# Performance work log

Hardware: AMD Instinct MI355X
Metric: run time of the kernel (lower is better)

Reference implementation:

```python
import jax, jax.numpy as jnp
import numpy as np
import math

GROUPS = 32
HEADS = 8
EPS_GN = 1e-5


def group_norm(x, w, b):
    # x: [B, C, H, W]; GroupNorm32 computes in float32
    B, C, H, W = x.shape
    xg = x.astype(jnp.float32).reshape(B, GROUPS, C // GROUPS, H, W)
    mu = xg.mean(axis=(2, 3, 4), keepdims=True)
    var = xg.var(axis=(2, 3, 4), keepdims=True)
    xn = (xg - mu) * jax.lax.rsqrt(var + EPS_GN)
    xn = xn.reshape(B, C, H, W)
    return (xn * w[None, :, None, None] + b[None, :, None, None]).astype(x.dtype)


def fresnel_interference(H, W, wavelength):
    ys, xs = jnp.meshgrid(jnp.arange(H, dtype=jnp.float32),
                          jnp.arange(W, dtype=jnp.float32), indexing='ij')
    pos = jnp.stack([ys, xs], axis=-1).reshape(-1, 2)  # [N, 2]
    diff = pos[None, :, :] - pos[:, None, :]           # [N, N, 2]
    dist = jnp.sqrt((diff ** 2).sum(-1) + 1e-8)        # [N, N]
    phase = 2.0 * math.pi * dist / (jnp.abs(wavelength) * H + 1e-6)
    return jnp.cos(phase)


def fresnel_attn(h, qkv_w, out_w, out_b, wavelength):
    B, C, H, W = h.shape
    N = H * W
    dh = C // HEADS
    scale = dh ** -0.5
    xf = h.reshape(B, C, N).transpose(0, 2, 1)                 # [B, N, C]
    qkv = xf @ qkv_w                                            # [B, N, 3C]
    q, k, v = jnp.split(qkv, 3, axis=-1)
    def heads(t):
        return t.reshape(B, N, HEADS, dh).transpose(0, 2, 1, 3)  # [B, Hh, N, dh]
    q, k, v = heads(q), heads(k), heads(v)
    dots = jnp.einsum('bhnd,bhmd->bhnm', q, k) * scale
    interference = fresnel_interference(H, W, wavelength)       # [N, N]
    dots = dots + interference[None, None] * 0.1
    attn = jax.nn.softmax(dots, axis=-1)
    out = jnp.einsum('bhnm,bhmd->bhnd', attn, v)
    out = out.transpose(0, 2, 1, 3).reshape(B, N, C)
    out = out @ out_w + out_b
    return out.transpose(0, 2, 1).reshape(B, C, H, W)


def cross_attn(h, context, q_w, k_w, v_w, out_w, out_b):
    B, C, H, W = h.shape
    N = H * W
    inner = q_w.shape[1]
    dh = inner // HEADS
    scale = dh ** -0.5
    xf = h.reshape(B, C, N).transpose(0, 2, 1)                 # [B, N, C]
    q = xf @ q_w                                                # [B, N, inner]
    k = context @ k_w                                           # [B, L, inner]
    v = context @ v_w
    L = context.shape[1]
    q = q.reshape(B, N, HEADS, dh).transpose(0, 2, 1, 3)
    k = k.reshape(B, L, HEADS, dh).transpose(0, 2, 1, 3)
    v = v.reshape(B, L, HEADS, dh).transpose(0, 2, 1, 3)
    attn = jax.nn.softmax(jnp.einsum('bhnd,bhld->bhnl', q, k) * scale, axis=-1)
    out = jnp.einsum('bhnl,bhld->bhnd', attn, v)
    out = out.transpose(0, 2, 1, 3).reshape(B, N, inner)
    out = out @ out_w + out_b
    return out.transpose(0, 2, 1).reshape(B, C, H, W)


def setup_inputs() -> dict:
    key = jax.random.key(0)
    ks = jax.random.split(key, 10)
    B, C, H, W = 4, 512, 32, 32
    ctx_len, ctx_dim = 77, 768
    s = lambda d: 1.0 / math.sqrt(d)
    return {
        'x': jax.random.normal(ks[0], (B, C, H, W), jnp.float32),
        'context': jax.random.normal(ks[1], (B, ctx_len, ctx_dim), jnp.float32),
        'gn1_w': jnp.ones((C,), jnp.float32),
        'gn1_b': jnp.zeros((C,), jnp.float32),
        'gn2_w': jnp.ones((C,), jnp.float32),
        'gn2_b': jnp.zeros((C,), jnp.float32),
        'fa_qkv_w': jax.random.normal(ks[2], (C, 3 * C), jnp.float32) * s(C),
        'fa_out_w': jax.random.normal(ks[3], (C, C), jnp.float32) * s(C),
        'fa_out_b': jnp.zeros((C,), jnp.float32),
        'wavelength': jnp.asarray(0.1, jnp.float32),
        'ca_q_w': jax.random.normal(ks[4], (C, 512), jnp.float32) * s(C),
        'ca_k_w': jax.random.normal(ks[5], (ctx_dim, 512), jnp.float32) * s(ctx_dim),
        'ca_v_w': jax.random.normal(ks[6], (ctx_dim, 512), jnp.float32) * s(ctx_dim),
        'ca_out_w': jax.random.normal(ks[7], (512, C), jnp.float32) * s(512),
        'ca_out_b': jnp.zeros((C,), jnp.float32),
    }


def reference(x, context, gn1_w, gn1_b, gn2_w, gn2_b,
              fa_qkv_w, fa_out_w, fa_out_b, wavelength,
              ca_q_w, ca_k_w, ca_v_w, ca_out_w, ca_out_b):
    h = group_norm(x, gn1_w, gn1_b)
    h = fresnel_attn(h, fa_qkv_w, fa_out_w, fa_out_b, wavelength)
    x = x + h
    h = group_norm(x, gn2_w, gn2_b)
    h = cross_attn(h, context, ca_q_w, ca_k_w, ca_v_w, ca_out_w, ca_out_b)
    return x + h
```

## Files before the change

kernel.cpp:

```cpp
#include <hip/hip_runtime.h>
#include <hip/hip_bf16.h>
#include <math.h>

#define B_    4
#define N_    1024
#define L_    77

typedef float f4 __attribute__((ext_vector_type(4)));
typedef short bf8 __attribute__((ext_vector_type(8)));
typedef short s4v __attribute__((ext_vector_type(4)));

#if __has_builtin(__builtin_amdgcn_exp2f)
#define EXP2(x) __builtin_amdgcn_exp2f(x)
#else
#define EXP2(x) exp2f(x)
#endif

typedef const __attribute__((address_space(1))) void* gas_t;
typedef __attribute__((address_space(3))) void* las_t;
#define GLL16(g, l) __builtin_amdgcn_global_load_lds((gas_t)(const void*)(g), (las_t)(void*)(l), 16, 0, 0)

__device__ __forceinline__ float fs(short s) {
    unsigned u = ((unsigned)(unsigned short)s) << 16;
    return __builtin_bit_cast(float, u);
}
__device__ __forceinline__ short sf(float f) {
    unsigned u = __builtin_bit_cast(unsigned, f);
    unsigned r = (u + 0x7FFF + ((u >> 16) & 1)) >> 16;
    return (short)r;
}
__device__ __forceinline__ bf8 zero8() { bf8 v; for (int i = 0; i < 8; ++i) v[i] = 0; return v; }
__device__ __forceinline__ f4 zerof4() { f4 v; for (int i = 0; i < 4; ++i) v[i] = 0.f; return v; }

#define MFMA(a, b, c) __builtin_amdgcn_mfma_f32_16x16x32_bf16((a), (b), (c), 0, 0, 0)

__device__ __forceinline__ void gn_body(const float* __restrict__ src,
                                        const float* __restrict__ w,
                                        const float* __restrict__ bs,
                                        short* __restrict__ dst, int g, int b)
{
    const float* xb = src + ((size_t)b * 512 + g * 16) * 1024;
    float s = 0.f, ss = 0.f;
    for (int l = threadIdx.x; l < 4096; l += 256) {
        float4 v = *(const float4*)(xb + l * 4);
        s += v.x + v.y + v.z + v.w;
        ss += v.x * v.x + v.y * v.y + v.z * v.z + v.w * v.w;
    }
    for (int off = 32; off; off >>= 1) {
        s  += __shfl_down(s,  off);
        ss += __shfl_down(ss, off);
    }
    __shared__ float sred[8], ssred[8];
    int wid = threadIdx.x >> 6;
    if ((threadIdx.x & 63) == 0) { sred[wid] = s; ssred[wid] = ss; }
    __syncthreads();
    if (threadIdx.x == 0) {
        float S = 0.f, SS = 0.f;
        for (int i = 0; i < 4; ++i) { S += sred[i]; SS += ssred[i]; }
        float mu = S * (1.f / 16384.f);
        float var = SS * (1.f / 16384.f) - mu * mu;
        sred[4] = mu; ssred[4] = rsqrtf(var + 1e-5f);
    }
    __syncthreads();
    float mu = sred[4], rs = ssred[4];

    int c4 = threadIdx.x & 3, nb = threadIdx.x >> 2;
    int c = g * 16 + c4 * 4;
    float4 wv = *(const float4*)(w + c);
    float4 bv = *(const float4*)(bs + c);
    for (int rep = 0; rep < 16; ++rep) {
        int n = rep * 64 + nb;
        float v0 = xb[(size_t)(c4 * 4 + 0) * 1024 + n];
        float v1 = xb[(size_t)(c4 * 4 + 1) * 1024 + n];
        float v2 = xb[(size_t)(c4 * 4 + 2) * 1024 + n];
        float v3 = xb[(size_t)(c4 * 4 + 3) * 1024 + n];
        s4v hb;
        hb[0] = sf((v0 - mu) * rs * wv.x + bv.x);
        hb[1] = sf((v1 - mu) * rs * wv.y + bv.y);
        hb[2] = sf((v2 - mu) * rs * wv.z + bv.z);
        hb[3] = sf((v3 - mu) * rs * wv.w + bv.w);
        *(s4v*)(dst + ((size_t)b * 1024 + n) * 512 + c) = hb;
    }
}

__device__ __forceinline__ void wtile(const float* __restrict__ in, short* __restrict__ out,
                                      int K, int J, int tile, int tid, float (*t)[33])
{
    int jt = J >> 5;
    int j0 = (tile % jt) * 32, k0 = (tile / jt) * 32;
    int tx = tid & 31, ty = tid >> 5;
#pragma unroll
    for (int i = 0; i < 4; ++i)
        t[ty + i * 8][tx] = in[(size_t)(k0 + ty + i * 8) * J + j0 + tx];
    __syncthreads();
#pragma unroll
    for (int i = 0; i < 4; ++i)
        out[(size_t)(j0 + ty + i * 8) * K + k0 + tx] = sf(t[tx][ty + i * 8]);
}

__global__ __launch_bounds__(256)
void prep_mega(const float* __restrict__ x, const float* __restrict__ gn1w,
               const float* __restrict__ gn1b, short* __restrict__ h1b,
               const float* __restrict__ wl, short* __restrict__ tab,
               float* __restrict__ gstat,
               const float* __restrict__ qkvw, short* __restrict__ qkvwT,
               const float* __restrict__ faow, short* __restrict__ faowT,
               const float* __restrict__ caqw, short* __restrict__ caqwT,
               const float* __restrict__ cakw, short* __restrict__ cakwT,
               const float* __restrict__ cavw, short* __restrict__ cavwT,
               const float* __restrict__ caow, short* __restrict__ caowT,
               const float* __restrict__ ctx, short* __restrict__ ctxb)
{
    __shared__ float tls[32][33];
    int bid = blockIdx.x, tid = threadIdx.x;
    if (bid < 128) { gn_body(x, gn1w, gn1b, h1b, bid & 31, bid >> 5); return; }
    bid -= 128;
    if (bid < 16) {
        if (bid == 0) gstat[tid] = 0.f;
        int idx = bid * 256 + tid;
        if (idx < 3969) {
            int i = idx / 63, j = idx - i * 63;
            float dy = (float)(i - 31), dx = (float)(j - 31);
            float dist = sqrtf(dy * dy + dx * dx + 1e-8f);
            float den = fabsf(wl[0]) * 32.0f + 1e-6f;
            tab[idx] = sf(0.1f * cosf(6.283185307179586f * dist / den) * 1.4426950408889634f);
        }
        return;
    }
    bid -= 16;
    if (bid < 768) { wtile(qkvw, qkvwT, 512, 1536, bid, tid, tls); return; }
    bid -= 768;
    if (bid < 256) { wtile(faow, faowT, 512, 512, bid, tid, tls); return; }
    bid -= 256;
    if (bid < 256) { wtile(caqw, caqwT, 512, 512, bid, tid, tls); return; }
    bid -= 256;
    if (bid < 384) { wtile(cakw, cakwT, 768, 512, bid, tid, tls); return; }
    bid -= 384;
    if (bid < 384) { wtile(cavw, cavwT, 768, 512, bid, tid, tls); return; }
    bid -= 384;
    if (bid < 256) { wtile(caow, caowT, 512, 512, bid, tid, tls); return; }
    bid -= 256;
    int base = bid * 1024 + tid * 4;
    float4 v = *(const float4*)(ctx + base);
    s4v o; o[0] = sf(v.x); o[1] = sf(v.y); o[2] = sf(v.z); o[3] = sf(v.w);
    *(s4v*)(ctxb + base) = o;
}

template<int EPI>
__device__ __forceinline__ void gemm_body(
    short* As, short* Ws, int j0, int m0, int b,
    const short* __restrict__ A, const short* __restrict__ Wt,
    const float* __restrict__ bias, const float* __restrict__ res,
    void* __restrict__ outv, void* __restrict__ out2v, float* __restrict__ gstat,
    int M, int K, int J, long aStride, long wStride, long oStride, long o2Stride)
{
    int tid = threadIdx.x, w = tid >> 6, lane = tid & 63;
    int lr = lane & 15, lg = lane >> 4;
    int wr = w >> 1, wc = w & 1;
    const short* Ab  = A  + (size_t)b * aStride;
    const short* Wtb = Wt + (size_t)b * wStride;

    int srow = lane >> 2, schk = (lane & 3) * 8;
    const short* agp  = Ab  + (size_t)(m0 + w * 16 + srow) * K + schk;
    const short* wgp0 = Wtb + (size_t)(j0 + w * 32 + srow) * K + schk;
    const short* wgp1 = Wtb + (size_t)(j0 + w * 32 + 16 + srow) * K + schk;
    short* alp  = As + w * 512;
    short* wlp0 = Ws + w * 1024;
    short* wlp1 = Ws + w * 1024 + 512;

    f4 acc[2][4];
#pragma unroll
    for (int i = 0; i < 2; ++i)
#pragma unroll
        for (int j = 0; j < 4; ++j) acc[i][j] = zerof4();

    GLL16(agp,  alp);
    GLL16(wgp0, wlp0);
    GLL16(wgp1, wlp1);
    __syncthreads();

    int nk = K >> 5;
    for (int t = 0; t < nk; ++t) {
        int bb = t & 1, nb2 = bb ^ 1;
        if (t + 1 < nk) {
            int ko = (t + 1) << 5;
            GLL16(agp + ko,  alp + nb2 * 2048);
            GLL16(wgp0 + ko, wlp0 + nb2 * 4096);
            GLL16(wgp1 + ko, wlp1 + nb2 * 4096);
        }
        bf8 af[2], bfr[4];
#pragma unroll
        for (int fi = 0; fi < 2; ++fi)
            af[fi] = *(const bf8*)(As + bb * 2048 + (wr * 32 + fi * 16 + lr) * 32 + lg * 8);
#pragma unroll
        for (int fj = 0; fj < 4; ++fj)
            bfr[fj] = *(const bf8*)(Ws + bb * 4096 + (wc * 64 + fj * 16 + lr) * 32 + lg * 8);
#pragma unroll
        for (int fi = 0; fi < 2; ++fi)
#pragma unroll
            for (int fj = 0; fj < 4; ++fj)
                acc[fi][fj] = MFMA(af[fi], bfr[fj], acc[fi][fj]);
        __syncthreads();
    }

    if (EPI == 1 || EPI == 2) {
        float* out = (float*)outv + (size_t)b * oStride;
        const float* rp = res + (size_t)b * oStride;
#pragma unroll
        for (int fi = 0; fi < 2; ++fi) {
            int mbase = m0 + wr * 32 + fi * 16 + lg * 4;
            float4 bq = *(const float4*)(bias + mbase);
            float bvr[4] = {bq.x, bq.y, bq.z, bq.w};
            float sg = 0.f, ssg = 0.f;
#pragma unroll
            for (int reg = 0; reg < 4; ++reg) {
                size_t ro = (size_t)(mbase + reg) * J + j0 + wc * 64;
#pragma unroll
                for (int fj = 0; fj < 4; ++fj) {
                    size_t idx = ro + fj * 16 + lr;
                    float v = acc[fi][fj][reg] + bvr[reg] + rp[idx];
                    out[idx] = v;
                    if (EPI == 2) { sg += v; ssg += v * v; }
                }
            }
            if (EPI == 2) {
#pragma unroll
                for (int off = 32; off; off >>= 1) {
                    sg  += __shfl_down(sg,  off);
                    ssg += __shfl_down(ssg, off);
                }
                if (lane == 0) {
                    int g = mbase >> 4;
                    atomicAdd(&gstat[b * 64 + g * 2], sg);
                    atomicAdd(&gstat[b * 64 + g * 2 + 1], ssg);
                }
            }
        }
    } else if (EPI == 3) {
        if (j0 < 1024) {
            short* out = (short*)outv + (size_t)b * oStride;
#pragma unroll
            for (int fi = 0; fi < 2; ++fi)
#pragma unroll
                for (int reg = 0; reg < 4; ++reg) {
                    int m = m0 + wr * 32 + fi * 16 + lg * 4 + reg;
#pragma unroll
                    for (int fj = 0; fj < 4; ++fj)
                        out[(size_t)m * 1024 + j0 + wc * 64 + fj * 16 + lr] = sf(acc[fi][fj][reg]);
                }
        } else {
            short* Vgp = (short*)out2v + (size_t)b * o2Stride;
#pragma unroll
            for (int fi = 0; fi < 2; ++fi) {
                int n = m0 + wr * 32 + fi * 16 + lg * 4;
#pragma unroll
                for (int fj = 0; fj < 4; ++fj) {
                    int dg = j0 - 1024 + wc * 64 + fj * 16 + lr;
                    s4v v;
#pragma unroll
                    for (int reg = 0; reg < 4; ++reg) v[reg] = sf(acc[fi][fj][reg]);
                    *(s4v*)(Vgp + (size_t)dg * 1024 + n) = v;
                }
            }
        }
    } else {
        if (j0 < 512) {
            short* out = (short*)outv + (size_t)b * oStride;
#pragma unroll
            for (int fi = 0; fi < 2; ++fi)
#pragma unroll
                for (int reg = 0; reg < 4; ++reg) {
                    int m = m0 + wr * 32 + fi * 16 + lg * 4 + reg;
                    if (m < M) {
#pragma unroll
                        for (int fj = 0; fj < 4; ++fj)
                            out[(size_t)m * 512 + j0 + wc * 64 + fj * 16 + lr] = sf(acc[fi][fj][reg]);
                    }
                }
        } else {
            short* vt = (short*)out2v + (size_t)b * o2Stride;
#pragma unroll
            for (int fi = 0; fi < 2; ++fi) {
                int l0 = m0 + wr * 32 + fi * 16 + lg * 4;
                if (l0 < 80) {
#pragma unroll
                    for (int fj = 0; fj < 4; ++fj) {
                        int dg = j0 - 512 + wc * 64 + fj * 16 + lr;
                        s4v v;
#pragma unroll
                        for (int reg = 0; reg < 4; ++reg) v[reg] = sf(acc[fi][fj][reg]);
                        *(s4v*)(vt + (size_t)dg * 80 + l0) = v;
                    }
                }
            }
        }
    }
}

template<int EPI>
__global__ __launch_bounds__(256)
void gemm_std(const short* __restrict__ A, const short* __restrict__ Wt,
              const float* __restrict__ bias, const float* __restrict__ res,
              void* __restrict__ outv, void* __restrict__ out2v, float* __restrict__ gstat,
              int M, int K, int J, long aStride, long wStride, long oStride, long o2Stride)
{
    __shared__ short As[2 * 64 * 32];
    __shared__ short Ws[2 * 128 * 32];
    gemm_body<EPI>(As, Ws, blockIdx.x * 128, blockIdx.y * 64, blockIdx.z,
                   A, Wt, bias, res, outv, out2v, gstat, M, K, J,
                   aStride, wStride, oStride, o2Stride);
}

__global__ __launch_bounds__(256)
void gemm_qkv_kv(const short* __restrict__ h1b, const short* __restrict__ qkvwT,
                 short* __restrict__ qkb, short* __restrict__ Vg,
                 const short* __restrict__ ctxb, const short* __restrict__ cakwT,
                 short* __restrict__ k2b, short* __restrict__ v2t)
{
    __shared__ short As[2 * 64 * 32];
    __shared__ short Ws[2 * 128 * 32];
    if (blockIdx.y < 16) {
        gemm_body<3>(As, Ws, blockIdx.x * 128, blockIdx.y * 64, blockIdx.z,
                     h1b, qkvwT, nullptr, nullptr, qkb, Vg, nullptr,
                     1024, 512, 1536, 524288L, 0L, 1048576L, 524288L);
    } else if (blockIdx.x < 8) {
        gemm_body<4>(As, Ws, blockIdx.x * 128, (blockIdx.y - 16) * 64, blockIdx.z,
                     ctxb, cakwT, nullptr, nullptr, k2b, v2t, nullptr,
                     77, 768, 1024, 59136L, 0L, 39424L, 40960L);
    }
}

__global__ __launch_bounds__(256)
void fresnel_attn_v3(const short* __restrict__ qkb, const short* __restrict__ Vg,
                     const short* __restrict__ tab, short* __restrict__ ao)
{
    int qb = blockIdx.x, h = blockIdx.y, b = blockIdx.z;
    int n0 = qb * 64;
    __shared__ short Ks[2][64][64];
    __shared__ short Vt[2][64][64];
    __shared__ short Ps[4][16][72];
    __shared__ short tabs[4032];
    int tid = threadIdx.x, w = tid >> 6, lane = tid & 63;
    int lr = lane & 15, lg = lane >> 4;
    const short* qp = qkb + (size_t)b * 1048576;
    const short* vp = Vg + ((size_t)b * 512 + h * 64) * 1024;

    for (int l = tid; l < 504; l += 256)
        *(bf8*)&tabs[l * 8] = *(const bf8*)(tab + l * 8);

    int q = n0 + w * 16 + lr;
    bf8 qf0 = *(const bf8*)(qp + (size_t)q * 1024 + h * 64 + lg * 8);
    bf8 qf1 = *(const bf8*)(qp + (size_t)q * 1024 + h * 64 + 32 + lg * 8);

    int sr0 = tid >> 3, sc0 = tid & 7;
    int sr1 = 32 + sr0;
    int sw0 = ((sc0 ^ (sr0 & 7))) * 8;
    int sw1 = ((sc0 ^ (sr1 & 7))) * 8;

    *(bf8*)&Ks[0][sr0][sw0] = *(const bf8*)(qp + (size_t)sr0 * 1024 + 512 + h * 64 + sc0 * 8);
    *(bf8*)&Ks[0][sr1][sw1] = *(const bf8*)(qp + (size_t)sr1 * 1024 + 512 + h * 64 + sc0 * 8);
    *(bf8*)&Vt[0][sr0][sw0] = *(const bf8*)(vp + (size_t)sr0 * 1024 + sc0 * 8);
    *(bf8*)&Vt[0][sr1][sw1] = *(const bf8*)(vp + (size_t)sr1 * 1024 + sc0 * 8);
    __syncthreads();

    float mrun = -1e30f, lrun = 0.f;
    f4 o[4];
#pragma unroll
    for (int i = 0; i < 4; ++i) o[i] = zerof4();

    int ybase = (q >> 5) + 31;
    int xbase = (q & 31) + 31 - lg * 4;
    int rsw = lr & 7;
    int rc0 = (lg ^ rsw) * 8;
    int rc1 = ((4 + lg) ^ rsw) * 8;

    for (int t = 0; t < 16; ++t) {
        int cur = t & 1;
        int m0 = t << 6;
        bool more = t < 15;
        bf8 nk0, nk1, nv0, nv1;
        if (more) {
            int m1 = m0 + 64;
            nk0 = *(const bf8*)(qp + (size_t)(m1 + sr0) * 1024 + 512 + h * 64 + sc0 * 8);
            nk1 = *(const bf8*)(qp + (size_t)(m1 + sr1) * 1024 + 512 + h * 64 + sc0 * 8);
            nv0 = *(const bf8*)(vp + (size_t)sr0 * 1024 + m1 + sc0 * 8);
            nv1 = *(const bf8*)(vp + (size_t)sr1 * 1024 + m1 + sc0 * 8);
        }

        f4 sa[4];
#pragma unroll
        for (int fj = 0; fj < 4; ++fj) sa[fj] = zerof4();
        __builtin_amdgcn_s_setprio(1);
#pragma unroll
        for (int fj = 0; fj < 4; ++fj)
            sa[fj] = MFMA(*(const bf8*)&Ks[cur][fj * 16 + lr][rc0], qf0, sa[fj]);
#pragma unroll
        for (int fj = 0; fj < 4; ++fj)
            sa[fj] = MFMA(*(const bf8*)&Ks[cur][fj * 16 + lr][rc1], qf1, sa[fj]);
        __builtin_amdgcn_s_setprio(0);

        int yb = ybase - (m0 >> 5);
        float pv[4][4];
        float tmax = -1e30f;
#pragma unroll
        for (int fj = 0; fj < 4; ++fj) {
            int rowoff = (yb - (fj >> 1)) * 63 + xbase - (fj & 1) * 16;
#pragma unroll
            for (int reg = 0; reg < 4; ++reg) {
                float t2 = fmaf(sa[fj][reg], 0.18033688011112042f, fs(tabs[rowoff - reg]));
                pv[fj][reg] = t2;
                tmax = fmaxf(tmax, t2);
            }
        }
        if (__any(tmax > mrun + 8.f)) {
            tmax = fmaxf(tmax, __shfl_xor(tmax, 16));
            tmax = fmaxf(tmax, __shfl_xor(tmax, 32));
            float mnew = fmaxf(mrun, tmax);
            float rsc = EXP2(mrun - mnew);
            mrun = mnew;
            lrun *= rsc;
#pragma unroll
            for (int fd = 0; fd < 4; ++fd)
#pragma unroll
                for (int reg = 0; reg < 4; ++reg) o[fd][reg] *= rsc;
        }
        float psum = 0.f;
#pragma unroll
        for (int fj = 0; fj < 4; ++fj) {
            float p0 = EXP2(pv[fj][0] - mrun);
            float p1 = EXP2(pv[fj][1] - mrun);
            float p2 = EXP2(pv[fj][2] - mrun);
            float p3 = EXP2(pv[fj][3] - mrun);
            psum += (p0 + p1) + (p2 + p3);
            int r01, r23;
            asm("v_cvt_pk_bf16_f32 %0, %1, %2" : "=v"(r01) : "v"(p0), "v"(p1));
            asm("v_cvt_pk_bf16_f32 %0, %1, %2" : "=v"(r23) : "v"(p2), "v"(p3));
            int2 pr; pr.x = r01; pr.y = r23;
            *(int2*)&Ps[w][lr][fj * 16 + lg * 4] = pr;
        }
        psum += __shfl_xor(psum, 16);
        psum += __shfl_xor(psum, 32);
        lrun += psum;

        bf8 pa0 = *(const bf8*)&Ps[w][lr][lg * 8];
        bf8 pa1 = *(const bf8*)&Ps[w][lr][32 + lg * 8];
        __builtin_amdgcn_s_setprio(1);
#pragma unroll
        for (int fd = 0; fd < 4; ++fd) {
            o[fd] = MFMA(*(const bf8*)&Vt[cur][fd * 16 + lr][rc0], pa0, o[fd]);
            o[fd] = MFMA(*(const bf8*)&Vt[cur][fd * 16 + lr][rc1], pa1, o[fd]);
        }
        __builtin_amdgcn_s_setprio(0);

        if (more) {
            int nb = cur ^ 1;
            *(bf8*)&Ks[nb][sr0][sw0] = nk0;
            *(bf8*)&Ks[nb][sr1][sw1] = nk1;
            *(bf8*)&Vt[nb][sr0][sw0] = nv0;
            *(bf8*)&Vt[nb][sr1][sw1] = nv1;
        }
        __syncthreads();
    }

    float inv = 1.f / lrun;
    size_t rb = ((size_t)b * N_ + q) * 512 + h * 64;
#pragma unroll
    for (int fd = 0; fd < 4; ++fd) {
        s4v ov;
#pragma unroll
        for (int reg = 0; reg < 4; ++reg) ov[reg] = sf(o[fd][reg] * inv);
        *(s4v*)(ao + rb + fd * 16 + lg * 4) = ov;
    }
}

__global__ __launch_bounds__(256)
void cross_attn_fused(const float* __restrict__ x1, const float* __restrict__ gstat,
                      const float* __restrict__ gn2w, const float* __restrict__ gn2b,
                      const short* __restrict__ qwT,
                      const short* __restrict__ k2, const short* __restrict__ v2t,
                      short* __restrict__ ao2)
{
    int qb = blockIdx.x, h = blockIdx.y, b = blockIdx.z;
    int n0 = qb * 64;
    __shared__ short hq[2][64][40];
    __shared__ short wq[2 * 64 * 32];
    __shared__ short Qs[64][72], Ks[96][72], Vt[64][104];
    __shared__ short Ps[4][16][104];
    __shared__ float smu[32], srs[32];
    int tid = threadIdx.x, w = tid >> 6, lane = tid & 63;
    int lr = lane & 15, lg = lane >> 4;

    if (tid < 32) {
        float S  = gstat[b * 64 + tid * 2];
        float SS = gstat[b * 64 + tid * 2 + 1];
        float mu = S * (1.f / 16384.f);
        float var = SS * (1.f / 16384.f) - mu * mu;
        smu[tid] = mu;
        srs[tid] = rsqrtf(var + 1e-5f);
    }

    for (int l = tid; l < 768; l += 256) {
        int m = l >> 3, dq = l & 7;
        bf8 v = zero8();
        if (m < L_) v = *(const bf8*)(k2 + ((size_t)b * L_ + m) * 512 + h * 64 + dq * 8);
        *(bf8*)&Ks[m][dq * 8] = v;
    }
    for (int l = tid; l < 768; l += 256) {
        int d = l / 12, cq = l % 12;
        bf8 v = zero8();
        if (cq < 10) v = *(const bf8*)(v2t + ((size_t)b * 512 + h * 64 + d) * 80 + cq * 8);
        *(bf8*)&Vt[d][cq * 8] = v;
    }

    int srow = lane >> 2, schk = (lane & 3) * 8;
    const short* wgp = qwT + (size_t)(h * 64 + w * 16 + srow) * 512 + schk;
    short* wlp = wq + w * 512;

    int cr = tid >> 4, cn = (tid & 15) * 4;
    const float* xp0 = x1 + ((size_t)b * 512 + cr) * 1024 + n0 + cn;
    const float* xp1 = xp0 + 16 * 1024;

    GLL16(wgp, wlp);
    float4 f0 = *(const float4*)(xp0);
    float4 f1 = *(const float4*)(xp1);
    float wv0 = gn2w[cr],      bv0 = gn2b[cr];
    float wv1 = gn2w[cr + 16], bv1 = gn2b[cr + 16];
    __syncthreads();
    {
        float mu0 = smu[0], rs0 = srs[0];
        float mu1 = smu[1], rs1 = srs[1];
        float a0 = rs0 * wv0, a1 = rs1 * wv1;
        float c0 = bv0 - mu0 * a0, c1 = bv1 - mu1 * a1;
#pragma unroll
        for (int i = 0; i < 4; ++i) {
            hq[0][cn + i][cr]      = sf(f0[i] * a0 + c0);
            hq[0][cn + i][cr + 16] = sf(f1[i] * a1 + c1);
        }
    }
    __syncthreads();

    f4 qacc[4];
#pragma unroll
    for (int j = 0; j < 4; ++j) qacc[j] = zerof4();
    for (int t = 0; t < 16; ++t) {
        int cur = t & 1, nb = cur ^ 1;
        bool more = t < 15;
        float4 nf0, nf1;
        float nw0, nb0, nw1, nb1;
        if (more) {
            int ko = (t + 1) << 5;
            GLL16(wgp + ko, wlp + nb * 2048);
            nf0 = *(const float4*)(xp0 + ko * 1024);
            nf1 = *(const float4*)(xp1 + ko * 1024);
            nw0 = gn2w[ko + cr];      nb0 = gn2b[ko + cr];
            nw1 = gn2w[ko + cr + 16]; nb1 = gn2b[ko + cr + 16];
        }
        bf8 af = *(const bf8*)&hq[cur][w * 16 + lr][lg * 8];
#pragma unroll
        for (int fj = 0; fj < 4; ++fj)
            qacc[fj] = MFMA(af, *(const bf8*)(wq + cur * 2048 + (fj * 16 + lr) * 32 + lg * 8), qacc[fj]);
        if (more) {
            int g0 = (t + 1) * 2, g1 = g0 + 1;
            float mu0 = smu[g0], rs0 = srs[g0];
            float mu1 = smu[g1], rs1 = srs[g1];
            float a0 = rs0 * nw0, a1 = rs1 * nw1;
            float c0 = nb0 - mu0 * a0, c1 = nb1 - mu1 * a1;
#pragma unroll
            for (int i = 0; i < 4; ++i) {
                hq[nb][cn + i][cr]      = sf(nf0[i] * a0 + c0);
                hq[nb][cn + i][cr + 16] = sf(nf1[i] * a1 + c1);
            }
        }
        __syncthreads();
    }
#pragma unroll
    for (int fj = 0; fj < 4; ++fj)
#pragma unroll
        for (int reg = 0; reg < 4; ++reg)
            Qs[w * 16 + lg * 4 + reg][fj * 16 + lr] = sf(qacc[fj][reg]);
    __syncthreads();

    f4 sacc[6];
#pragma unroll
    for (int fj = 0; fj < 6; ++fj) sacc[fj] = zerof4();
    __builtin_amdgcn_s_setprio(1);
#pragma unroll
    for (int kc = 0; kc < 2; ++kc) {
        bf8 aq = *(const bf8*)&Qs[w * 16 + lr][kc * 32 + lg * 8];
#pragma unroll
        for (int fj = 0; fj < 6; ++fj)
            sacc[fj] = MFMA(aq, *(const bf8*)&Ks[fj * 16 + lr][kc * 32 + lg * 8], sacc[fj]);
    }
    __builtin_amdgcn_s_setprio(0);

    float rinv[4];
#pragma unroll
    for (int reg = 0; reg < 4; ++reg) {
        float sv[6];
#pragma unroll
        for (int fj = 0; fj < 6; ++fj) {
            int m = fj * 16 + lr;
            sv[fj] = (m < L_) ? sacc[fj][reg] * 0.125f : -30000.f;
        }
        float mx = sv[0];
#pragma unroll
        for (int fj = 1; fj < 6; ++fj) mx = fmaxf(mx, sv[fj]);
#pragma unroll
        for (int off = 1; off < 16; off <<= 1) mx = fmaxf(mx, __shfl_xor(mx, off));
        float psum = 0.f;
#pragma unroll
        for (int fj = 0; fj < 6; ++fj) {
            float p = __expf(sv[fj] - mx);
            psum += p;
            Ps[w][lg * 4 + reg][fj * 16 + lr] = sf(p);
        }
#pragma unroll
        for (int off = 1; off < 16; off <<= 1) psum += __shfl_xor(psum, off);
        rinv[reg] = 1.f / psum;
    }
    __syncthreads();

    f4 o[4];
#pragma unroll
    for (int fd = 0; fd < 4; ++fd) o[fd] = zerof4();
    __builtin_amdgcn_s_setprio(1);
#pragma unroll
    for (int kc = 0; kc < 3; ++kc) {
        bf8 ap = *(const bf8*)&Ps[w][lr][kc * 32 + lg * 8];
#pragma unroll
        for (int fd = 0; fd < 4; ++fd)
            o[fd] = MFMA(ap, *(const bf8*)&Vt[fd * 16 + lr][kc * 32 + lg * 8], o[fd]);
    }
    __builtin_amdgcn_s_setprio(0);

#pragma unroll
    for (int reg = 0; reg < 4; ++reg) {
        size_t rb = ((size_t)b * N_ + n0 + w * 16 + lg * 4 + reg) * 512 + h * 64;
#pragma unroll
        for (int fd = 0; fd < 4; ++fd)
            ao2[rb + fd * 16 + lr] = sf(o[fd][reg] * rinv[reg]);
    }
}

extern "C" void kernel_launch(void* const* d_in, const int* in_sizes, int n_in,
                              void* d_out, int out_size, void* d_ws, size_t ws_size,
                              hipStream_t stream)
{
    const float* x    = (const float*)d_in[0];
    const float* ctx  = (const float*)d_in[1];
    const float* gn1w = (const float*)d_in[2];
    const float* gn1b = (const float*)d_in[3];
    const float* gn2w = (const float*)d_in[4];
    const float* gn2b = (const float*)d_in[5];
    const float* qkvw = (const float*)d_in[6];
    const float* faow = (const float*)d_in[7];
    const float* faob = (const float*)d_in[8];
    const float* wl   = (const float*)d_in[9];
    const float* caqw = (const float*)d_in[10];
    const float* cakw = (const float*)d_in[11];
    const float* cavw = (const float*)d_in[12];
    const float* caow = (const float*)d_in[13];
    const float* caob = (const float*)d_in[14];
    float* out = (float*)d_out;
    char* ws = (char*)d_ws;

    float* x1    = (float*)(ws + 0);
    short* qkb   = (short*)(ws + 8388608);
    short* Vg    = (short*)(ws + 16777216);
    short* h1b   = (short*)(ws + 20971520);
    short* ao    = (short*)(ws + 25165824);
    float* gstat = (float*)(ws + 29360128);
    short* qkvwT = (short*)(ws + 33554432);
    short* faowT = (short*)(ws + 35127296);
    short* caqwT = (short*)(ws + 35651584);
    short* cakwT = (short*)(ws + 36175872);
    short* cavwT = (short*)(ws + 36962304);
    short* caowT = (short*)(ws + 37748736);
    short* k2b   = (short*)(ws + 38273024);
    short* v2t   = (short*)(ws + 38588416);
    short* ctxb  = (short*)(ws + 38916096);
    short* tab   = (short*)(ws + 39389184);

    prep_mega<<<2679, 256, 0, stream>>>(x, gn1w, gn1b, h1b,
                                        wl, tab, gstat, qkvw, qkvwT, faow, faowT,
                                        caqw, caqwT, cakw, cakwT, cavw, cavwT,
                                        caow, caowT, ctx, ctxb);
    gemm_qkv_kv<<<dim3(12, 18, 4), 256, 0, stream>>>(
        h1b, qkvwT, qkb, Vg, ctxb, cakwT, k2b, v2t);
    fresnel_attn_v3<<<dim3(16, 8, 4), 256, 0, stream>>>(qkb, Vg, tab, ao);
    gemm_std<2><<<dim3(8, 8, 4), 256, 0, stream>>>(
        faowT, ao, faob, x, x1, nullptr, gstat, 512, 512, 1024,
        0L, 524288L, 524288L, 0L);
    cross_attn_fused<<<dim3(16, 8, 4), 256, 0, stream>>>(
        x1, gstat, gn2w, gn2b, caqwT, k2b, v2t, ao);
    gemm_std<1><<<dim3(8, 8, 4), 256, 0, stream>>>(
        caowT, ao, caob, x1, out, nullptr, nullptr, 512, 512, 1024,
        0L, 524288L, 524288L, 0L);
}
```

Baseline: 203.1 us.

## Split fresnel attention over key halves with last-block merge; widen QKV GEMM tiles

The fresnel attention kernel now splits each query block's key range into two halves, so twice as many blocks run. Each half writes unnormalised partial outputs plus running max and sum to a workspace, and the last block to finish merges both halves, ordered by an atomic counter. Separately, the QKV/KV projection GEMM moves to 128x128 tiles, which gives more reuse per block but fewer blocks. The split adds extra global traffic, fences and a bf16 round-trip for the partials, in exchange for better CU occupancy on a grid that was only 512 blocks.

```diff
diff --git a/kernel.cpp b/kernel.cpp
--- a/kernel.cpp
+++ b/kernel.cpp
@@ -102,7 +102,7 @@
 void prep_mega(const float* __restrict__ x, const float* __restrict__ gn1w,
                const float* __restrict__ gn1b, short* __restrict__ h1b,
                const float* __restrict__ wl, short* __restrict__ tab,
-               float* __restrict__ gstat,
+               float* __restrict__ gstat, int* __restrict__ flags,
                const float* __restrict__ qkvw, short* __restrict__ qkvwT,
                const float* __restrict__ faow, short* __restrict__ faowT,
                const float* __restrict__ caqw, short* __restrict__ caqwT,
@@ -117,6 +117,7 @@
     bid -= 128;
     if (bid < 16) {
         if (bid == 0) gstat[tid] = 0.f;
+        if (bid == 1) { flags[tid] = 0; flags[tid + 256] = 0; }
         int idx = bid * 256 + tid;
         if (idx < 3969) {
             int i = idx / 63, j = idx - i * 63;
@@ -151,8 +152,8 @@
     short* As, short* Ws, int j0, int m0, int b,
     const short* __restrict__ A, const short* __restrict__ Wt,
     const float* __restrict__ bias, const float* __restrict__ res,
-    void* __restrict__ outv, void* __restrict__ out2v, float* __restrict__ gstat,
-    int M, int K, int J, long aStride, long wStride, long oStride, long o2Stride)
+    void* __restrict__ outv, float* __restrict__ gstat,
+    int M, int K, int J, long aStride, long wStride, long oStride)
 {
     int tid = threadIdx.x, w = tid >> 6, lane = tid & 63;
     int lr = lane & 15, lg = lane >> 4;
@@ -203,47 +204,117 @@
         __syncthreads();
     }
 
-    if (EPI == 1 || EPI == 2) {
-        float* out = (float*)outv + (size_t)b * oStride;
-        const float* rp = res + (size_t)b * oStride;
-#pragma unroll
-        for (int fi = 0; fi < 2; ++fi) {
-            int mbase = m0 + wr * 32 + fi * 16 + lg * 4;
-            float4 bq = *(const float4*)(bias + mbase);
-            float bvr[4] = {bq.x, bq.y, bq.z, bq.w};
-            float sg = 0.f, ssg = 0.f;
-#pragma unroll
-            for (int reg = 0; reg < 4; ++reg) {
-                size_t ro = (size_t)(mbase + reg) * J + j0 + wc * 64;
-#pragma unroll
-                for (int fj = 0; fj < 4; ++fj) {
-                    size_t idx = ro + fj * 16 + lr;
-                    float v = acc[fi][fj][reg] + bvr[reg] + rp[idx];
-                    out[idx] = v;
-                    if (EPI == 2) { sg += v; ssg += v * v; }
-                }
+    float* out = (float*)outv + (size_t)b * oStride;
+    const float* rp = res + (size_t)b * oStride;
+#pragma unroll
+    for (int fi = 0; fi < 2; ++fi) {
+        int mbase = m0 + wr * 32 + fi * 16 + lg * 4;
+        float4 bq = *(const float4*)(bias + mbase);
+        float bvr[4] = {bq.x, bq.y, bq.z, bq.w};
+        float sg = 0.f, ssg = 0.f;
+#pragma unroll
+        for (int reg = 0; reg < 4; ++reg) {
+            size_t ro = (size_t)(mbase + reg) * J + j0 + wc * 64;
+#pragma unroll
+            for (int fj = 0; fj < 4; ++fj) {
+                size_t idx = ro + fj * 16 + lr;
+                float v = acc[fi][fj][reg] + bvr[reg] + rp[idx];
+                out[idx] = v;
+                if (EPI == 2) { sg += v; ssg += v * v; }
             }
-            if (EPI == 2) {
-#pragma unroll
-                for (int off = 32; off; off >>= 1) {
-                    sg  += __shfl_down(sg,  off);
-                    ssg += __shfl_down(ssg, off);
-                }
-                if (lane == 0) {
-                    int g = mbase >> 4;
-                    atomicAdd(&gstat[b * 64 + g * 2], sg);
-                    atomicAdd(&gstat[b * 64 + g * 2 + 1], ssg);
-                }
+        }
+        if (EPI == 2) {
+#pragma unroll
+            for (int off = 32; off; off >>= 1) {
+                sg  += __shfl_down(sg,  off);
+                ssg += __shfl_down(ssg, off);
             }
-        }
-    } else if (EPI == 3) {
+            if (lane == 0) {
+                int g = mbase >> 4;
+                atomicAdd(&gstat[b * 64 + g * 2], sg);
+                atomicAdd(&gstat[b * 64 + g * 2 + 1], ssg);
+            }
+        }
+    }
+}
+
+template<int EPI>
+__global__ __launch_bounds__(256)
+void gemm_std(const short* __restrict__ A, const short* __restrict__ Wt,
+              const float* __restrict__ bias, const float* __restrict__ res,
+              void* __restrict__ outv, float* __restrict__ gstat,
+              int M, int K, int J, long aStride, long wStride, long oStride)
+{
+    __shared__ short As[2 * 64 * 32];
+    __shared__ short Ws[2 * 128 * 32];
+    gemm_body<EPI>(As, Ws, blockIdx.x * 128, blockIdx.y * 64, blockIdx.z,
+                   A, Wt, bias, res, outv, gstat, M, K, J,
+                   aStride, wStride, oStride);
+}
+
+template<int EPI>
+__device__ __forceinline__ void gemm_body128(
+    short* As, short* Ws, int j0, int m0, int b,
+    const short* __restrict__ A, const short* __restrict__ Wt,
+    void* __restrict__ outv, void* __restrict__ out2v,
+    int M, int K, long aStride, long oStride, long o2Stride)
+{
+    int tid = threadIdx.x, w = tid >> 6, lane = tid & 63;
+    int lr = lane & 15, lg = lane >> 4;
+    int wr = w >> 1, wc = w & 1;
+    const short* Ab = A + (size_t)b * aStride;
+
+    int srow = lane >> 2, schk = (lane & 3) * 8;
+    const short* agp0 = Ab + (size_t)(m0 + w * 32 + srow) * K + schk;
+    const short* agp1 = agp0 + (size_t)16 * K;
+    const short* wgp0 = Wt + (size_t)(j0 + w * 32 + srow) * K + schk;
+    const short* wgp1 = wgp0 + (size_t)16 * K;
+    short* alp0 = As + w * 1024;
+    short* alp1 = alp0 + 512;
+    short* wlp0 = Ws + w * 1024;
+    short* wlp1 = wlp0 + 512;
+
+    f4 acc[4][4];
+#pragma unroll
+    for (int i = 0; i < 4; ++i)
+#pragma unroll
+        for (int j = 0; j < 4; ++j) acc[i][j] = zerof4();
+
+    GLL16(agp0, alp0); GLL16(agp1, alp1);
+    GLL16(wgp0, wlp0); GLL16(wgp1, wlp1);
+    __syncthreads();
+
+    int nk = K >> 5;
+    for (int t = 0; t < nk; ++t) {
+        int bb = (t & 1) * 4096, nxt = 4096 - bb;
+        if (t + 1 < nk) {
+            int ko = (t + 1) << 5;
+            GLL16(agp0 + ko, alp0 + nxt); GLL16(agp1 + ko, alp1 + nxt);
+            GLL16(wgp0 + ko, wlp0 + nxt); GLL16(wgp1 + ko, wlp1 + nxt);
+        }
+        bf8 af[4], bfr[4];
+#pragma unroll
+        for (int fi = 0; fi < 4; ++fi)
+            af[fi] = *(const bf8*)(As + bb + (wr * 64 + fi * 16 + lr) * 32 + lg * 8);
+#pragma unroll
+        for (int fj = 0; fj < 4; ++fj)
+            bfr[fj] = *(const bf8*)(Ws + bb + (wc * 64 + fj * 16 + lr) * 32 + lg * 8);
+#pragma unroll
+        for (int fi = 0; fi < 4; ++fi)
+#pragma unroll
+            for (int fj = 0; fj < 4; ++fj)
+                acc[fi][fj] = MFMA(af[fi], bfr[fj], acc[fi][fj]);
+        __syncthreads();
+    }
+
+    if (EPI == 3) {
         if (j0 < 1024) {
             short* out = (short*)outv + (size_t)b * oStride;
 #pragma unroll
-            for (int fi = 0; fi < 2; ++fi)
+            for (int fi = 0; fi < 4; ++fi)
 #pragma unroll
                 for (int reg = 0; reg < 4; ++reg) {
-                    int m = m0 + wr * 32 + fi * 16 + lg * 4 + reg;
+                    int m = m0 + wr * 64 + fi * 16 + lg * 4 + reg;
 #pragma unroll
                     for (int fj = 0; fj < 4; ++fj)
                         out[(size_t)m * 1024 + j0 + wc * 64 + fj * 16 + lr] = sf(acc[fi][fj][reg]);
@@ -251,8 +322,8 @@
         } else {
             short* Vgp = (short*)out2v + (size_t)b * o2Stride;
 #pragma unroll
-            for (int fi = 0; fi < 2; ++fi) {
-                int n = m0 + wr * 32 + fi * 16 + lg * 4;
+            for (int fi = 0; fi < 4; ++fi) {
+                int n = m0 + wr * 64 + fi * 16 + lg * 4;
 #pragma unroll
                 for (int fj = 0; fj < 4; ++fj) {
                     int dg = j0 - 1024 + wc * 64 + fj * 16 + lr;
@@ -267,10 +338,10 @@
         if (j0 < 512) {
             short* out = (short*)outv + (size_t)b * oStride;
 #pragma unroll
-            for (int fi = 0; fi < 2; ++fi)
+            for (int fi = 0; fi < 4; ++fi)
 #pragma unroll
                 for (int reg = 0; reg < 4; ++reg) {
-                    int m = m0 + wr * 32 + fi * 16 + lg * 4 + reg;
+                    int m = m0 + wr * 64 + fi * 16 + lg * 4 + reg;
                     if (m < M) {
 #pragma unroll
                         for (int fj = 0; fj < 4; ++fj)
@@ -280,8 +351,8 @@
         } else {
             short* vt = (short*)out2v + (size_t)b * o2Stride;
 #pragma unroll
-            for (int fi = 0; fi < 2; ++fi) {
-                int l0 = m0 + wr * 32 + fi * 16 + lg * 4;
+            for (int fi = 0; fi < 4; ++fi) {
+                int l0 = m0 + wr * 64 + fi * 16 + lg * 4;
                 if (l0 < 80) {
 #pragma unroll
                     for (int fj = 0; fj < 4; ++fj) {
@@ -297,49 +368,40 @@
     }
 }
 
-template<int EPI>
-__global__ __launch_bounds__(256)
-void gemm_std(const short* __restrict__ A, const short* __restrict__ Wt,
-              const float* __restrict__ bias, const float* __restrict__ res,
-              void* __restrict__ outv, void* __restrict__ out2v, float* __restrict__ gstat,
-              int M, int K, int J, long aStride, long wStride, long oStride, long o2Stride)
-{
-    __shared__ short As[2 * 64 * 32];
-    __shared__ short Ws[2 * 128 * 32];
-    gemm_body<EPI>(As, Ws, blockIdx.x * 128, blockIdx.y * 64, blockIdx.z,
-                   A, Wt, bias, res, outv, out2v, gstat, M, K, J,
-                   aStride, wStride, oStride, o2Stride);
-}
-
 __global__ __launch_bounds__(256)
 void gemm_qkv_kv(const short* __restrict__ h1b, const short* __restrict__ qkvwT,
                  short* __restrict__ qkb, short* __restrict__ Vg,
                  const short* __restrict__ ctxb, const short* __restrict__ cakwT,
                  short* __restrict__ k2b, short* __restrict__ v2t)
 {
-    __shared__ short As[2 * 64 * 32];
+    __shared__ short As[2 * 128 * 32];
     __shared__ short Ws[2 * 128 * 32];
-    if (blockIdx.y < 16) {
-        gemm_body<3>(As, Ws, blockIdx.x * 128, blockIdx.y * 64, blockIdx.z,
-                     h1b, qkvwT, nullptr, nullptr, qkb, Vg, nullptr,
-                     1024, 512, 1536, 524288L, 0L, 1048576L, 524288L);
+    if (blockIdx.y < 8) {
+        gemm_body128<3>(As, Ws, blockIdx.x * 128, blockIdx.y * 128, blockIdx.z,
+                        h1b, qkvwT, qkb, Vg,
+                        1024, 512, 524288L, 1048576L, 524288L);
     } else if (blockIdx.x < 8) {
-        gemm_body<4>(As, Ws, blockIdx.x * 128, (blockIdx.y - 16) * 64, blockIdx.z,
-                     ctxb, cakwT, nullptr, nullptr, k2b, v2t, nullptr,
-                     77, 768, 1024, 59136L, 0L, 39424L, 40960L);
+        gemm_body128<4>(As, Ws, blockIdx.x * 128, 0, blockIdx.z,
+                        ctxb, cakwT, k2b, v2t,
+                        77, 768, 59136L, 39424L, 40960L);
     }
 }
 
 __global__ __launch_bounds__(256)
-void fresnel_attn_v3(const short* __restrict__ qkb, const short* __restrict__ Vg,
-                     const short* __restrict__ tab, short* __restrict__ ao)
-{
-    int qb = blockIdx.x, h = blockIdx.y, b = blockIdx.z;
+void fresnel_attn_v4(const short* __restrict__ qkb, const short* __restrict__ Vg,
+                     const short* __restrict__ tab, short* __restrict__ ao,
+                     short* __restrict__ aop, float* __restrict__ msc,
+                     float* __restrict__ lsc, int* __restrict__ flags)
+{
+    int qb = blockIdx.x >> 1, half = blockIdx.x & 1;
+    int h = blockIdx.y, b = blockIdx.z;
     int n0 = qb * 64;
+    int kbase = half * 512;
     __shared__ short Ks[2][64][64];
     __shared__ short Vt[2][64][64];
     __shared__ short Ps[4][16][72];
     __shared__ short tabs[4032];
+    __shared__ int cflag;
     int tid = threadIdx.x, w = tid >> 6, lane = tid & 63;
     int lr = lane & 15, lg = lane >> 4;
     const short* qp = qkb + (size_t)b * 1048576;
@@ -357,10 +419,10 @@
     int sw0 = ((sc0 ^ (sr0 & 7))) * 8;
     int sw1 = ((sc0 ^ (sr1 & 7))) * 8;
 
-    *(bf8*)&Ks[0][sr0][sw0] = *(const bf8*)(qp + (size_t)sr0 * 1024 + 512 + h * 64 + sc0 * 8);
-    *(bf8*)&Ks[0][sr1][sw1] = *(const bf8*)(qp + (size_t)sr1 * 1024 + 512 + h * 64 + sc0 * 8);
-    *(bf8*)&Vt[0][sr0][sw0] = *(const bf8*)(vp + (size_t)sr0 * 1024 + sc0 * 8);
-    *(bf8*)&Vt[0][sr1][sw1] = *(const bf8*)(vp + (size_t)sr1 * 1024 + sc0 * 8);
+    *(bf8*)&Ks[0][sr0][sw0] = *(const bf8*)(qp + (size_t)(kbase + sr0) * 1024 + 512 + h * 64 + sc0 * 8);
+    *(bf8*)&Ks[0][sr1][sw1] = *(const bf8*)(qp + (size_t)(kbase + sr1) * 1024 + 512 + h * 64 + sc0 * 8);
+    *(bf8*)&Vt[0][sr0][sw0] = *(const bf8*)(vp + (size_t)sr0 * 1024 + kbase + sc0 * 8);
+    *(bf8*)&Vt[0][sr1][sw1] = *(const bf8*)(vp + (size_t)sr1 * 1024 + kbase + sc0 * 8);
     __syncthreads();
 
     float mrun = -1e30f, lrun = 0.f;
@@ -374,10 +436,10 @@
     int rc0 = (lg ^ rsw) * 8;
     int rc1 = ((4 + lg) ^ rsw) * 8;
 
-    for (int t = 0; t < 16; ++t) {
+    for (int t = 0; t < 8; ++t) {
         int cur = t & 1;
-        int m0 = t << 6;
-        bool more = t < 15;
+        int m0 = kbase + (t << 6);
+        bool more = t < 7;
         bf8 nk0, nk1, nv0, nv1;
         if (more) {
             int m1 = m0 + 64;
@@ -462,14 +524,47 @@
         __syncthreads();
     }
 
-    float inv = 1.f / lrun;
-    size_t rb = ((size_t)b * N_ + q) * 512 + h * 64;
+    size_t pb = (size_t)half * 2097152 + ((size_t)b * 1024 + q) * 512 + h * 64;
 #pragma unroll
     for (int fd = 0; fd < 4; ++fd) {
         s4v ov;
 #pragma unroll
-        for (int reg = 0; reg < 4; ++reg) ov[reg] = sf(o[fd][reg] * inv);
-        *(s4v*)(ao + rb + fd * 16 + lg * 4) = ov;
+        for (int reg = 0; reg < 4; ++reg) ov[reg] = sf(o[fd][reg]);
+        *(s4v*)(aop + pb + fd * 16 + lg * 4) = ov;
+    }
+    int sidx = ((half * 4 + b) * 8 + h) * 1024 + q;
+    msc[sidx] = mrun;
+    lsc[sidx] = lrun;
+
+    __syncthreads();
+    int fidx = (b * 8 + h) * 16 + qb;
+    if (tid == 0) {
+        __threadfence();
+        cflag = atomicAdd(&flags[fidx], 1);
+    }
+    __syncthreads();
+    if (cflag == 1) {
+        __threadfence();
+        for (int l = tid; l < 512; l += 256) {
+            int qq = l >> 3, dq = l & 7;
+            int q2 = n0 + qq;
+            int i0 = ((0 * 4 + b) * 8 + h) * 1024 + q2;
+            int i1 = ((1 * 4 + b) * 8 + h) * 1024 + q2;
+            float m0v = msc[i0], l0v = lsc[i0];
+            float m1v = msc[i1], l1v = lsc[i1];
+            float mm = fmaxf(m0v, m1v);
+            float w0 = EXP2(m0v - mm), w1 = EXP2(m1v - mm);
+            float inv = 1.f / (l0v * w0 + l1v * w1);
+            w0 *= inv; w1 *= inv;
+            size_t base = ((size_t)b * 1024 + q2) * 512 + h * 64 + dq * 8;
+            bf8 a0 = *(const bf8*)(aop + base);
+            bf8 a1 = *(const bf8*)(aop + 2097152 + base);
+            bf8 r;
+#pragma unroll
+            for (int i = 0; i < 8; ++i)
+                r[i] = sf(fs(a0[i]) * w0 + fs(a1[i]) * w1);
+            *(bf8*)(ao + base) = r;
+        }
     }
 }
 
@@ -669,31 +764,36 @@
     short* Vg    = (short*)(ws + 16777216);
     short* h1b   = (short*)(ws + 20971520);
     short* ao    = (short*)(ws + 25165824);
-    float* gstat = (float*)(ws + 29360128);
-    short* qkvwT = (short*)(ws + 33554432);
-    short* faowT = (short*)(ws + 35127296);
-    short* caqwT = (short*)(ws + 35651584);
-    short* cakwT = (short*)(ws + 36175872);
-    short* cavwT = (short*)(ws + 36962304);
-    short* caowT = (short*)(ws + 37748736);
-    short* k2b   = (short*)(ws + 38273024);
-    short* v2t   = (short*)(ws + 38588416);
-    short* ctxb  = (short*)(ws + 38916096);
-    short* tab   = (short*)(ws + 39389184);
+    short* aop   = (short*)(ws + 29360128);
+    float* msc   = (float*)(ws + 37748736);
+    float* lsc   = (float*)(ws + 38010880);
+    float* gstat = (float*)(ws + 38273024);
+    int*   flags = (int*)  (ws + 38274048);
+    short* qkvwT = (short*)(ws + 38277120);
+    short* faowT = (short*)(ws + 39849984);
+    short* caqwT = (short*)(ws + 40374272);
+    short* cakwT = (short*)(ws + 40898560);
+    short* cavwT = (short*)(ws + 41684992);
+    short* caowT = (short*)(ws + 42471424);
+    short* k2b   = (short*)(ws + 42995712);
+    short* v2t   = (short*)(ws + 43311104);
+    short* ctxb  = (short*)(ws + 43638784);
+    short* tab   = (short*)(ws + 44111872);
 
     prep_mega<<<2679, 256, 0, stream>>>(x, gn1w, gn1b, h1b,
-                                        wl, tab, gstat, qkvw, qkvwT, faow, faowT,
-                                        caqw, caqwT, cakw, cakwT, cavw, cavwT,
-                                        caow, caowT, ctx, ctxb);
-    gemm_qkv_kv<<<dim3(12, 18, 4), 256, 0, stream>>>(
+                                        wl, tab, gstat, flags, qkvw, qkvwT,
+                                        faow, faowT, caqw, caqwT, cakw, cakwT,
+                                        cavw, cavwT, caow, caowT, ctx, ctxb);
+    gemm_qkv_kv<<<dim3(12, 9, 4), 256, 0, stream>>>(
         h1b, qkvwT, qkb, Vg, ctxb, cakwT, k2b, v2t);
-    fresnel_attn_v3<<<dim3(16, 8, 4), 256, 0, stream>>>(qkb, Vg, tab, ao);
+    fresnel_attn_v4<<<dim3(32, 8, 4), 256, 0, stream>>>(
+        qkb, Vg, tab, ao, aop, msc, lsc, flags);
     gemm_std<2><<<dim3(8, 8, 4), 256, 0, stream>>>(
-        faowT, ao, faob, x, x1, nullptr, gstat, 512, 512, 1024,
-        0L, 524288L, 524288L, 0L);
+        faowT, ao, faob, x, x1, gstat, 512, 512, 1024,
+        0L, 524288L, 524288L);
     cross_attn_fused<<<dim3(16, 8, 4), 256, 0, stream>>>(
         x1, gstat, gn2w, gn2b, caqwT, k2b, v2t, ao);
     gemm_std<1><<<dim3(8, 8, 4), 256, 0, stream>>>(
-        caowT, ao, caob, x1, out, nullptr, nullptr, 512, 512, 1024,
-        0L, 524288L, 524288L, 0L);
-}
+        caowT, ao, caob, x1, out, nullptr, 512, 512, 1024,
+        0L, 524288L, 524288L);
+}
```

Result: slower. 332.3 us (+63.6%).
